# Performance work log

Hardware: AMD Instinct MI355X
Metric: run time of the kernel (lower is better)

Reference implementation:

```python
import jax, jax.numpy as jnp
import numpy as np

N = 100000
E = 1600000

def _graphconv(x, src, dst, W, b):
    # DGL GraphConv, norm='both', in_feats > out_feats path: transform then aggregate.
    ones = jnp.ones((E,), dtype=x.dtype)
    out_deg = jax.ops.segment_sum(ones, src, num_segments=N)
    in_deg = jax.ops.segment_sum(ones, dst, num_segments=N)
    out_norm = jax.lax.rsqrt(jnp.clip(out_deg, 1.0))  # D_out^{-1/2}
    in_norm = jax.lax.rsqrt(jnp.clip(in_deg, 1.0))    # D_in^{-1/2}
    h = (x * out_norm[:, None]) @ W                    # [N, out_feats]
    msg = h[src]                                       # gather over edges [E, out_feats]
    agg = jax.ops.segment_sum(msg, dst, num_segments=N)
    return agg * in_norm[:, None] + b


def setup_inputs() -> dict:
    key = jax.random.key(0)
    k1, k2, k3, k4, k5 = jax.random.split(key, 5)
    features = jax.random.normal(k1, (N, 256), dtype=jnp.float32)
    src = jax.random.randint(k2, (E,), 0, N, dtype=jnp.int32)
    dst = jax.random.randint(k3, (E,), 0, N, dtype=jnp.int32)
    # Xavier-uniform like DGL's GraphConv reset_parameters
    lim1 = float(np.sqrt(6.0 / (256 + 64)))
    lim2 = float(np.sqrt(6.0 / (64 + 40)))
    W1 = jax.random.uniform(k4, (256, 64), jnp.float32, -lim1, lim1)
    W2 = jax.random.uniform(k5, (64, 40), jnp.float32, -lim2, lim2)
    b1 = jnp.zeros((64,), jnp.float32)
    b2 = jnp.zeros((40,), jnp.float32)
    return {"features": features, "src": src, "dst": dst,
            "W1": W1, "b1": b1, "W2": W2, "b2": b2}


def reference(features, src, dst, W1, b1, W2, b2):
    x = _graphconv(features, src, dst, W1, b1)
    x = _graphconv(x, src, dst, W2, b2)
    return x
```

## Files before the change

### kernel.cpp

```cpp
#include <hip/hip_runtime.h>

#define N_NODES 100000
#define N_EDGES 1600000
#define BSH 7
#define NBUCK 782
#define BMASK 127
#define HBLK 512
#define CAP 4096


__global__ __launch_bounds__(256) void coarse_hist_kernel(
    const int* __restrict__ src, const int* __restrict__ dst,
    int* __restrict__ gHD, int* __restrict__ gHS) {
    __shared__ int hd[NBUCK], hs[NBUCK];
    for (int i = threadIdx.x; i < NBUCK; i += 256) { hd[i] = 0; hs[i] = 0; }
    __syncthreads();
    for (int e = blockIdx.x * 256 + threadIdx.x; e < N_EDGES; e += HBLK * 256) {
        atomicAdd(&hd[dst[e] >> BSH], 1);
        atomicAdd(&hs[src[e] >> BSH], 1);
    }
    __syncthreads();
    for (int i = threadIdx.x; i < NBUCK; i += 256) {
        if (hd[i]) atomicAdd(&gHD[i], hd[i]);
        if (hs[i]) atomicAdd(&gHS[i], hs[i]);
    }
}


__global__ __launch_bounds__(1024) void coarse_scan_kernel(
    const int* __restrict__ gHD, const int* __restrict__ gHS,
    int* __restrict__ dBase, int* __restrict__ sBase) {
    __shared__ int sd[1024], se[1024];
    int t = threadIdx.x;
    int vd = (t < NBUCK) ? gHD[t] : 0;
    int vs = (t < NBUCK) ? gHS[t] : 0;
    sd[t] = vd; se[t] = vs;
    __syncthreads();
    for (int s = 1; s < 1024; s <<= 1) {
        int ud = (t >= s) ? sd[t - s] : 0;
        int us = (t >= s) ? se[t - s] : 0;
        __syncthreads();
        sd[t] += ud; se[t] += us;
        __syncthreads();
    }
    if (t < NBUCK) { dBase[t] = sd[t] - vd; sBase[t] = se[t] - vs; }
    if (t == 0) { dBase[NBUCK] = N_EDGES; sBase[NBUCK] = N_EDGES; }
}


__global__ __launch_bounds__(256) void scatter_both_kernel(
    const int* __restrict__ src, const int* __restrict__ dst,
    const int* __restrict__ dBase, const int* __restrict__ sBase,
    int* __restrict__ dRes, int* __restrict__ sRes,
    int* __restrict__ bpack, unsigned char* __restrict__ bslo) {
    __shared__ int hd[NBUCK], hs[NBUCK], curD[NBUCK], curS[NBUCK];
    for (int i = threadIdx.x; i < NBUCK; i += 256) { hd[i] = 0; hs[i] = 0; }
    __syncthreads();
    for (int e = blockIdx.x * 256 + threadIdx.x; e < N_EDGES; e += HBLK * 256) {
        atomicAdd(&hd[dst[e] >> BSH], 1);
        atomicAdd(&hs[src[e] >> BSH], 1);
    }
    __syncthreads();
    for (int i = threadIdx.x; i < NBUCK; i += 256) {
        int cd = hd[i];
        curD[i] = dBase[i] + (cd ? atomicAdd(&dRes[i], cd) : 0);
        int cs = hs[i];
        curS[i] = sBase[i] + (cs ? atomicAdd(&sRes[i], cs) : 0);
    }
    __syncthreads();
    for (int e = blockIdx.x * 256 + threadIdx.x; e < N_EDGES; e += HBLK * 256) {
        int s = src[e];
        int d = dst[e];
        int pd = atomicAdd(&curD[d >> BSH], 1);
        bpack[pd] = (s << BSH) | (d & BMASK);
        int ps = atomicAdd(&curS[s >> BSH], 1);
        bslo[ps] = (unsigned char)(s & BMASK);
    }
}


__global__ __launch_bounds__(256) void fine_src_kernel(
    const int* __restrict__ sBase, const unsigned char* __restrict__ bslo,
    float* __restrict__ onorm) {
    __shared__ int hist[128];
    int t = threadIdx.x, b = blockIdx.x;
    int lo = sBase[b], hi = sBase[b + 1];
    if (t < 128) hist[t] = 0;
    __syncthreads();
    for (int p = lo + t; p < hi; p += 256) atomicAdd(&hist[bslo[p]], 1);
    __syncthreads();
    int node = b * 128 + t;
    if (t < 128 && node < N_NODES) onorm[node] = 1.0f / sqrtf((float)max(hist[t], 1));
}


__global__ __launch_bounds__(128) void gemm1_kernel(
    const float* __restrict__ x, const float* __restrict__ W,
    const float* __restrict__ onorm, float* __restrict__ h, int n) {
    __shared__ float As[16][128];
    __shared__ float Ws[16][68];
    const int tid = threadIdx.x;
    const int tx = tid & 7;
    const int ry = tid >> 3;
    const int rowBase = blockIdx.x * 128;

    const int lr = tid >> 2;
    const int kq = (tid & 3) * 4;
    const int wk = tid >> 3;
    const int wc = (tid & 7) * 8;

    float4 va[4], vw0, vw1;

    auto load_regs = [&](int k0) {
#pragma unroll
        for (int p = 0; p < 4; ++p) {
            int row = rowBase + p * 32 + lr;
            va[p] = (row < n) ? *(const float4*)(x + (size_t)row * 256 + k0 + kq)
                              : make_float4(0.f, 0.f, 0.f, 0.f);
        }
        vw0 = *(const float4*)(W + (size_t)wk * 64 + wc);
        vw1 = *(const float4*)(W + (size_t)wk * 64 + wc + 4);
    };
    auto load_regs_w = [&](int k0) {
#pragma unroll
        for (int p = 0; p < 4; ++p) {
            int row = rowBase + p * 32 + lr;
            va[p] = (row < n) ? *(const float4*)(x + (size_t)row * 256 + k0 + kq)
                              : make_float4(0.f, 0.f, 0.f, 0.f);
        }
        vw0 = *(const float4*)(W + (size_t)(k0 + wk) * 64 + wc);
        vw1 = *(const float4*)(W + (size_t)(k0 + wk) * 64 + wc + 4);
    };

    float acc[8][8] = {};

    load_regs(0);
    for (int k0 = 0; k0 < 256; k0 += 16) {
#pragma unroll
        for (int p = 0; p < 4; ++p) {
            int r = p * 32 + lr;
            As[kq + 0][r] = va[p].x;
            As[kq + 1][r] = va[p].y;
            As[kq + 2][r] = va[p].z;
            As[kq + 3][r] = va[p].w;
        }
        *(float4*)&Ws[wk][wc] = vw0;
        *(float4*)&Ws[wk][wc + 4] = vw1;
        __syncthreads();
        if (k0 + 16 < 256) load_regs_w(k0 + 16);
#pragma unroll
        for (int k = 0; k < 16; ++k) {
            float4 b0 = *(const float4*)&Ws[k][tx * 8];
            float4 b1 = *(const float4*)&Ws[k][tx * 8 + 4];
            float4 a0 = *(const float4*)&As[k][ry * 8];
            float4 a1 = *(const float4*)&As[k][ry * 8 + 4];
            float av[8] = {a0.x, a0.y, a0.z, a0.w, a1.x, a1.y, a1.z, a1.w};
            float bv[8] = {b0.x, b0.y, b0.z, b0.w, b1.x, b1.y, b1.z, b1.w};
#pragma unroll
            for (int i = 0; i < 8; ++i)
#pragma unroll
                for (int j = 0; j < 8; ++j) acc[i][j] += av[i] * bv[j];
        }
        __syncthreads();
    }
#pragma unroll
    for (int i = 0; i < 8; ++i) {
        int row = rowBase + ry * 8 + i;
        if (row < n) {
            float s = onorm[row];
            *(float4*)(h + (size_t)row * 64 + tx * 8) =
                make_float4(acc[i][0] * s, acc[i][1] * s, acc[i][2] * s, acc[i][3] * s);
            *(float4*)(h + (size_t)row * 64 + tx * 8 + 4) =
                make_float4(acc[i][4] * s, acc[i][5] * s, acc[i][6] * s, acc[i][7] * s);
        }
    }
}


__global__ __launch_bounds__(512) void agg64_fused_kernel(
    const int* __restrict__ dBase, const int* __restrict__ bpack,
    const float* __restrict__ h, float* __restrict__ agg, float* __restrict__ inorm) {
    __shared__ int lsrc[CAP];
    __shared__ int hist[128], scn[128], cur[128];
    const int tid = threadIdx.x;
    const int b = blockIdx.x;
    const int lo = dBase[b];
    const int hi = min(dBase[b + 1], lo + CAP);
    if (tid < 128) hist[tid] = 0;
    __syncthreads();
    for (int p = lo + tid; p < hi; p += 512) atomicAdd(&hist[bpack[p] & BMASK], 1);
    __syncthreads();
    int v = (tid < 128) ? hist[tid] : 0;
    if (tid < 128) scn[tid] = v;
    __syncthreads();
    for (int s = 1; s < 128; s <<= 1) {
        int u = 0;
        if (tid < 128 && tid >= s) u = scn[tid - s];
        __syncthreads();
        if (tid < 128 && tid >= s) scn[tid] += u;
        __syncthreads();
    }
    if (tid < 128) {
        int excl = scn[tid] - v;
        scn[tid] = excl;
        cur[tid] = excl;
        int node = b * 128 + tid;
        if (node < N_NODES) inorm[node] = 1.0f / sqrtf((float)max(v, 1));
    }
    __syncthreads();
    for (int p = lo + tid; p < hi; p += 512) {
        int pk = bpack[p];
        int pos = atomicAdd(&cur[pk & BMASK], 1);
        lsrc[pos] = pk >> BSH;
    }
    __syncthreads();

    const int w = tid >> 6, lane = tid & 63, q = lane >> 4, f = lane & 15;
    for (int nn = w; nn < 128; nn += 8) {
        int node = b * 128 + nn;
        if (node >= N_NODES) break;
        int beg = scn[nn];
        int end = beg + hist[nn];
        float4 a0 = {0.f, 0.f, 0.f, 0.f}, a1 = {0.f, 0.f, 0.f, 0.f};
        int j = beg;
        for (; j + 8 <= end; j += 8) {
            int s0 = lsrc[j + q], s1 = lsrc[j + 4 + q];
            float4 v0 = *((const float4*)(h + (size_t)s0 * 64) + f);
            float4 v1 = *((const float4*)(h + (size_t)s1 * 64) + f);
            a0.x += v0.x; a0.y += v0.y; a0.z += v0.z; a0.w += v0.w;
            a1.x += v1.x; a1.y += v1.y; a1.z += v1.z; a1.w += v1.w;
        }
        for (; j + 4 <= end; j += 4) {
            int s0 = lsrc[j + q];
            float4 v0 = *((const float4*)(h + (size_t)s0 * 64) + f);
            a0.x += v0.x; a0.y += v0.y; a0.z += v0.z; a0.w += v0.w;
        }
        if (j + q < end) {
            int s0 = lsrc[j + q];
            float4 v0 = *((const float4*)(h + (size_t)s0 * 64) + f);
            a0.x += v0.x; a0.y += v0.y; a0.z += v0.z; a0.w += v0.w;
        }
        a0.x += a1.x; a0.y += a1.y; a0.z += a1.z; a0.w += a1.w;
        a0.x += __shfl_xor(a0.x, 16); a0.y += __shfl_xor(a0.y, 16);
        a0.z += __shfl_xor(a0.z, 16); a0.w += __shfl_xor(a0.w, 16);
        a0.x += __shfl_xor(a0.x, 32); a0.y += __shfl_xor(a0.y, 32);
        a0.z += __shfl_xor(a0.z, 32); a0.w += __shfl_xor(a0.w, 32);
        if (q == 0) ((float4*)(agg + (size_t)node * 64))[f] = a0;
    }
}


__global__ __launch_bounds__(256) void gemm2_kernel(
    const float* __restrict__ agg, const float* __restrict__ W2,
    const float* __restrict__ b1, const float* __restrict__ inorm,
    const float* __restrict__ onorm, float* __restrict__ h2, int n) {
    const int lane = threadIdx.x & 63;
    const int wid = __builtin_amdgcn_readfirstlane(threadIdx.x >> 6);
    const int rowBase = (blockIdx.x * 4 + wid) * 8;
    const int cl = lane < 40 ? lane : 39;

    float w[64];
#pragma unroll
    for (int k = 0; k < 64; ++k) w[k] = W2[k * 40 + cl];

    float c2 = 0.f;
#pragma unroll
    for (int k = 0; k < 64; ++k) c2 += b1[k] * w[k];

#pragma unroll
    for (int r = 0; r < 8; ++r) {
        int row = rowBase + r;
        if (row < n) {
            const float* ar = agg + (size_t)row * 64;
            float acc = 0.f;
#pragma unroll
            for (int k = 0; k < 64; ++k) acc += ar[k] * w[k];
            float so = onorm[row];
            float s12 = inorm[row] * so;
            if (lane < 40) h2[(size_t)row * 40 + lane] = acc * s12 + so * c2;
        }
    }
}


__global__ __launch_bounds__(512) void agg40_fused_kernel(
    const int* __restrict__ dBase, const int* __restrict__ bpack,
    const float* __restrict__ h2, const float* __restrict__ b2,
    float* __restrict__ out) {
    __shared__ int lsrc[CAP];
    __shared__ int hist[128], scn[128], cur[128];
    const int tid = threadIdx.x;
    const int b = blockIdx.x;
    const int lo = dBase[b];
    const int hi = min(dBase[b + 1], lo + CAP);
    if (tid < 128) hist[tid] = 0;
    __syncthreads();
    for (int p = lo + tid; p < hi; p += 512) atomicAdd(&hist[bpack[p] & BMASK], 1);
    __syncthreads();
    int v = (tid < 128) ? hist[tid] : 0;
    if (tid < 128) scn[tid] = v;
    __syncthreads();
    for (int s = 1; s < 128; s <<= 1) {
        int u = 0;
        if (tid < 128 && tid >= s) u = scn[tid - s];
        __syncthreads();
        if (tid < 128 && tid >= s) scn[tid] += u;
        __syncthreads();
    }
    if (tid < 128) {
        int excl = scn[tid] - v;
        scn[tid] = excl;
        cur[tid] = excl;
    }
    __syncthreads();
    for (int p = lo + tid; p < hi; p += 512) {
        int pk = bpack[p];
        int pos = atomicAdd(&cur[pk & BMASK], 1);
        lsrc[pos] = pk >> BSH;
    }
    __syncthreads();

    const int w = tid >> 6, lane = tid & 63, q = lane >> 4, f = lane & 15;
    const bool act = (f < 10);
    float4 vb = make_float4(0.f, 0.f, 0.f, 0.f);
    if (act) vb = ((const float4*)b2)[f];
    for (int nn = w; nn < 128; nn += 8) {
        int node = b * 128 + nn;
        if (node >= N_NODES) break;
        int beg = scn[nn];
        int end = beg + hist[nn];
        float4 a0 = {0.f, 0.f, 0.f, 0.f}, a1 = {0.f, 0.f, 0.f, 0.f};
        int j = beg;
        for (; j + 8 <= end; j += 8) {
            int s0 = lsrc[j + q], s1 = lsrc[j + 4 + q];
            if (act) {
                float4 v0 = *((const float4*)(h2 + (size_t)s0 * 40) + f);
                float4 v1 = *((const float4*)(h2 + (size_t)s1 * 40) + f);
                a0.x += v0.x; a0.y += v0.y; a0.z += v0.z; a0.w += v0.w;
                a1.x += v1.x; a1.y += v1.y; a1.z += v1.z; a1.w += v1.w;
            }
        }
        for (; j + 4 <= end; j += 4) {
            int s0 = lsrc[j + q];
            if (act) {
                float4 v0 = *((const float4*)(h2 + (size_t)s0 * 40) + f);
                a0.x += v0.x; a0.y += v0.y; a0.z += v0.z; a0.w += v0.w;
            }
        }
        if (j + q < end && act) {
            int s0 = lsrc[j + q];
            float4 v0 = *((const float4*)(h2 + (size_t)s0 * 40) + f);
            a0.x += v0.x; a0.y += v0.y; a0.z += v0.z; a0.w += v0.w;
        }
        a0.x += a1.x; a0.y += a1.y; a0.z += a1.z; a0.w += a1.w;
        a0.x += __shfl_xor(a0.x, 16); a0.y += __shfl_xor(a0.y, 16);
        a0.z += __shfl_xor(a0.z, 16); a0.w += __shfl_xor(a0.w, 16);
        a0.x += __shfl_xor(a0.x, 32); a0.y += __shfl_xor(a0.y, 32);
        a0.z += __shfl_xor(a0.z, 32); a0.w += __shfl_xor(a0.w, 32);
        if (q == 0 && act) {
            float s = 1.0f / sqrtf((float)max(hist[nn], 1));
            float4 r;
            r.x = a0.x * s + vb.x; r.y = a0.y * s + vb.y;
            r.z = a0.z * s + vb.z; r.w = a0.w * s + vb.w;
            ((float4*)(out + (size_t)node * 40))[f] = r;
        }
    }
}

extern "C" void kernel_launch(void* const* d_in, const int* in_sizes, int n_in,
                              void* d_out, int out_size, void* d_ws, size_t ws_size,
                              hipStream_t stream) {
    const float* x  = (const float*)d_in[0];
    const int* src  = (const int*)d_in[1];
    const int* dst  = (const int*)d_in[2];
    const float* W1 = (const float*)d_in[3];
    const float* b1 = (const float*)d_in[4];
    const float* W2 = (const float*)d_in[5];
    const float* b2 = (const float*)d_in[6];
    float* out = (float*)d_out;

    char* wsb = (char*)d_ws;
    size_t off = 0;
    auto alloc = [&](size_t bytes) { char* p = wsb + off; off += (bytes + 255) & ~size_t(255); return p; };

    int*   zeroed = (int*)  alloc(4 * NBUCK * 4);
    int*   gHD    = zeroed;
    int*   gHS    = zeroed + NBUCK;
    int*   dRes   = zeroed + 2 * NBUCK;
    int*   sRes   = zeroed + 3 * NBUCK;
    int*   dBase  = (int*)  alloc((NBUCK + 1) * 4);
    int*   sBase  = (int*)  alloc((NBUCK + 1) * 4);
    float* onorm  = (float*)alloc(N_NODES * 4);
    float* inorm  = (float*)alloc(N_NODES * 4);
    int*   bpack  = (int*)  alloc((size_t)N_EDGES * 4);
    unsigned char* bslo = (unsigned char*)alloc(N_EDGES);
    float* h1     = (float*)alloc((size_t)N_NODES * 64 * 4);
    float* agg1   = (float*)alloc((size_t)N_NODES * 64 * 4);
    float* h2 = h1;

    hipMemsetAsync(zeroed, 0, 4 * NBUCK * 4, stream);

    coarse_hist_kernel<<<HBLK, 256, 0, stream>>>(src, dst, gHD, gHS);
    coarse_scan_kernel<<<1, 1024, 0, stream>>>(gHD, gHS, dBase, sBase);
    scatter_both_kernel<<<HBLK, 256, 0, stream>>>(src, dst, dBase, sBase, dRes, sRes,
                                                  bpack, bslo);
    fine_src_kernel<<<NBUCK, 256, 0, stream>>>(sBase, bslo, onorm);

    gemm1_kernel<<<(N_NODES + 127) / 128, 128, 0, stream>>>(x, W1, onorm, h1, N_NODES);

    agg64_fused_kernel<<<NBUCK, 512, 0, stream>>>(dBase, bpack, h1, agg1, inorm);

    gemm2_kernel<<<(N_NODES + 31) / 32, 256, 0, stream>>>(agg1, W2, b1, inorm, onorm, h2, N_NODES);

    agg40_fused_kernel<<<NBUCK, 512, 0, stream>>>(dBase, bpack, h2, b2, out);
}
```

Measured before the change: 432.8 us.

## Use per-block histograms with scan, LDS atomic aggregation, and wider gemm1 blocks

Counting-sort offsets now come from per-block histograms and a column-wise scan kernel, so the scatter no longer recomputes histograms or takes global atomic reservations. The scatter order becomes deterministic, and the extra HBLK*NBUCK buffers cost more memory traffic. Both aggregation kernels drop the in-LDS bucket sort and per-node warp reduction. They now accumulate edge messages straight into padded shared-memory accumulators with float atomics, which also removes the CAP truncation. gemm1 moves to 256 threads with an 8x4 per-thread tile and no register prefetch.

Measured after the change: 1.396 ms. 3.23x slower.

```diff
diff --git a/kernel.cpp b/kernel.cpp
--- a/kernel.cpp
+++ b/kernel.cpp
@@ -6,12 +6,13 @@
 #define NBUCK 782
 #define BMASK 127
 #define HBLK 512
-#define CAP 4096
+#define PAD64 65
+#define PAD40 41
 
 
 __global__ __launch_bounds__(256) void coarse_hist_kernel(
     const int* __restrict__ src, const int* __restrict__ dst,
-    int* __restrict__ gHD, int* __restrict__ gHS) {
+    int* __restrict__ dHist, int* __restrict__ sHist) {
     __shared__ int hd[NBUCK], hs[NBUCK];
     for (int i = threadIdx.x; i < NBUCK; i += 256) { hd[i] = 0; hs[i] = 0; }
     __syncthreads();
@@ -20,10 +21,35 @@
         atomicAdd(&hs[src[e] >> BSH], 1);
     }
     __syncthreads();
+    size_t base = (size_t)blockIdx.x * NBUCK;
     for (int i = threadIdx.x; i < NBUCK; i += 256) {
-        if (hd[i]) atomicAdd(&gHD[i], hd[i]);
-        if (hs[i]) atomicAdd(&gHS[i], hs[i]);
-    }
+        dHist[base + i] = hd[i];
+        sHist[base + i] = hs[i];
+    }
+}
+
+
+__global__ __launch_bounds__(512) void scan_blocks_kernel(
+    const int* __restrict__ dHist, const int* __restrict__ sHist,
+    int* __restrict__ dOfs, int* __restrict__ sOfs,
+    int* __restrict__ gHD, int* __restrict__ gHS) {
+    __shared__ int sd[512], se[512];
+    const int i = blockIdx.x;
+    const int t = threadIdx.x;
+    int vd = dHist[(size_t)t * NBUCK + i];
+    int vs = sHist[(size_t)t * NBUCK + i];
+    sd[t] = vd; se[t] = vs;
+    __syncthreads();
+    for (int s = 1; s < 512; s <<= 1) {
+        int ud = (t >= s) ? sd[t - s] : 0;
+        int us = (t >= s) ? se[t - s] : 0;
+        __syncthreads();
+        sd[t] += ud; se[t] += us;
+        __syncthreads();
+    }
+    dOfs[(size_t)t * NBUCK + i] = sd[t] - vd;
+    sOfs[(size_t)t * NBUCK + i] = se[t] - vs;
+    if (t == 511) { gHD[i] = sd[511]; gHS[i] = se[511]; }
 }
 
 
@@ -51,21 +77,13 @@
 __global__ __launch_bounds__(256) void scatter_both_kernel(
     const int* __restrict__ src, const int* __restrict__ dst,
     const int* __restrict__ dBase, const int* __restrict__ sBase,
-    int* __restrict__ dRes, int* __restrict__ sRes,
+    const int* __restrict__ dOfs, const int* __restrict__ sOfs,
     int* __restrict__ bpack, unsigned char* __restrict__ bslo) {
-    __shared__ int hd[NBUCK], hs[NBUCK], curD[NBUCK], curS[NBUCK];
-    for (int i = threadIdx.x; i < NBUCK; i += 256) { hd[i] = 0; hs[i] = 0; }
-    __syncthreads();
-    for (int e = blockIdx.x * 256 + threadIdx.x; e < N_EDGES; e += HBLK * 256) {
-        atomicAdd(&hd[dst[e] >> BSH], 1);
-        atomicAdd(&hs[src[e] >> BSH], 1);
-    }
-    __syncthreads();
+    __shared__ int curD[NBUCK], curS[NBUCK];
+    size_t obase = (size_t)blockIdx.x * NBUCK;
     for (int i = threadIdx.x; i < NBUCK; i += 256) {
-        int cd = hd[i];
-        curD[i] = dBase[i] + (cd ? atomicAdd(&dRes[i], cd) : 0);
-        int cs = hs[i];
-        curS[i] = sBase[i] + (cs ? atomicAdd(&sRes[i], cs) : 0);
+        curD[i] = dBase[i] + dOfs[obase + i];
+        curS[i] = sBase[i] + sOfs[obase + i];
     }
     __syncthreads();
     for (int e = blockIdx.x * 256 + threadIdx.x; e < N_EDGES; e += HBLK * 256) {
@@ -94,158 +112,103 @@
 }
 
 
-__global__ __launch_bounds__(128) void gemm1_kernel(
+__global__ __launch_bounds__(256) void gemm1_kernel(
     const float* __restrict__ x, const float* __restrict__ W,
     const float* __restrict__ onorm, float* __restrict__ h, int n) {
     __shared__ float As[16][128];
     __shared__ float Ws[16][68];
     const int tid = threadIdx.x;
-    const int tx = tid & 7;
-    const int ry = tid >> 3;
+    const int tx = tid & 15;
+    const int ry = tid >> 4;
     const int rowBase = blockIdx.x * 128;
 
-    const int lr = tid >> 2;
-    const int kq = (tid & 3) * 4;
-    const int wk = tid >> 3;
-    const int wc = (tid & 7) * 8;
-
-    float4 va[4], vw0, vw1;
-
-    auto load_regs = [&](int k0) {
-#pragma unroll
-        for (int p = 0; p < 4; ++p) {
-            int row = rowBase + p * 32 + lr;
-            va[p] = (row < n) ? *(const float4*)(x + (size_t)row * 256 + k0 + kq)
-                              : make_float4(0.f, 0.f, 0.f, 0.f);
-        }
-        vw0 = *(const float4*)(W + (size_t)wk * 64 + wc);
-        vw1 = *(const float4*)(W + (size_t)wk * 64 + wc + 4);
-    };
-    auto load_regs_w = [&](int k0) {
-#pragma unroll
-        for (int p = 0; p < 4; ++p) {
-            int row = rowBase + p * 32 + lr;
-            va[p] = (row < n) ? *(const float4*)(x + (size_t)row * 256 + k0 + kq)
-                              : make_float4(0.f, 0.f, 0.f, 0.f);
-        }
-        vw0 = *(const float4*)(W + (size_t)(k0 + wk) * 64 + wc);
-        vw1 = *(const float4*)(W + (size_t)(k0 + wk) * 64 + wc + 4);
-    };
-
-    float acc[8][8] = {};
-
-    load_regs(0);
+    const int lr = tid >> 1;
+    const int kq = (tid & 1) * 8;
+    const int wk = tid >> 4;
+    const int wc = (tid & 15) * 4;
+
+    const int row = rowBase + lr;
+    const bool rv = (row < n);
+    const float* xr = x + (size_t)row * 256;
+
+    float acc[8][4] = {};
+
     for (int k0 = 0; k0 < 256; k0 += 16) {
-#pragma unroll
-        for (int p = 0; p < 4; ++p) {
-            int r = p * 32 + lr;
-            As[kq + 0][r] = va[p].x;
-            As[kq + 1][r] = va[p].y;
-            As[kq + 2][r] = va[p].z;
-            As[kq + 3][r] = va[p].w;
-        }
-        *(float4*)&Ws[wk][wc] = vw0;
-        *(float4*)&Ws[wk][wc + 4] = vw1;
-        __syncthreads();
-        if (k0 + 16 < 256) load_regs_w(k0 + 16);
+        float4 v0 = make_float4(0.f, 0.f, 0.f, 0.f), v1 = v0;
+        if (rv) {
+            v0 = *(const float4*)(xr + k0 + kq);
+            v1 = *(const float4*)(xr + k0 + kq + 4);
+        }
+        *(float4*)&Ws[wk][wc] = *(const float4*)(W + (size_t)(k0 + wk) * 64 + wc);
+        As[kq + 0][lr] = v0.x;
+        As[kq + 1][lr] = v0.y;
+        As[kq + 2][lr] = v0.z;
+        As[kq + 3][lr] = v0.w;
+        As[kq + 4][lr] = v1.x;
+        As[kq + 5][lr] = v1.y;
+        As[kq + 6][lr] = v1.z;
+        As[kq + 7][lr] = v1.w;
+        __syncthreads();
 #pragma unroll
         for (int k = 0; k < 16; ++k) {
-            float4 b0 = *(const float4*)&Ws[k][tx * 8];
-            float4 b1 = *(const float4*)&Ws[k][tx * 8 + 4];
+            float4 b = *(const float4*)&Ws[k][tx * 4];
             float4 a0 = *(const float4*)&As[k][ry * 8];
             float4 a1 = *(const float4*)&As[k][ry * 8 + 4];
             float av[8] = {a0.x, a0.y, a0.z, a0.w, a1.x, a1.y, a1.z, a1.w};
-            float bv[8] = {b0.x, b0.y, b0.z, b0.w, b1.x, b1.y, b1.z, b1.w};
+            float bv[4] = {b.x, b.y, b.z, b.w};
 #pragma unroll
             for (int i = 0; i < 8; ++i)
 #pragma unroll
-                for (int j = 0; j < 8; ++j) acc[i][j] += av[i] * bv[j];
+                for (int j = 0; j < 4; ++j) acc[i][j] += av[i] * bv[j];
         }
         __syncthreads();
     }
 #pragma unroll
     for (int i = 0; i < 8; ++i) {
-        int row = rowBase + ry * 8 + i;
-        if (row < n) {
-            float s = onorm[row];
-            *(float4*)(h + (size_t)row * 64 + tx * 8) =
+        int r = rowBase + ry * 8 + i;
+        if (r < n) {
+            float s = onorm[r];
+            *(float4*)(h + (size_t)r * 64 + tx * 4) =
                 make_float4(acc[i][0] * s, acc[i][1] * s, acc[i][2] * s, acc[i][3] * s);
-            *(float4*)(h + (size_t)row * 64 + tx * 8 + 4) =
-                make_float4(acc[i][4] * s, acc[i][5] * s, acc[i][6] * s, acc[i][7] * s);
-        }
-    }
-}
-
-
-__global__ __launch_bounds__(512) void agg64_fused_kernel(
+        }
+    }
+}
+
+
+__global__ __launch_bounds__(512) void agg64_kernel(
     const int* __restrict__ dBase, const int* __restrict__ bpack,
     const float* __restrict__ h, float* __restrict__ agg, float* __restrict__ inorm) {
-    __shared__ int lsrc[CAP];
-    __shared__ int hist[128], scn[128], cur[128];
+    __shared__ float accL[128 * PAD64];
+    __shared__ int degL[128];
     const int tid = threadIdx.x;
     const int b = blockIdx.x;
-    const int lo = dBase[b];
-    const int hi = min(dBase[b + 1], lo + CAP);
-    if (tid < 128) hist[tid] = 0;
-    __syncthreads();
-    for (int p = lo + tid; p < hi; p += 512) atomicAdd(&hist[bpack[p] & BMASK], 1);
-    __syncthreads();
-    int v = (tid < 128) ? hist[tid] : 0;
-    if (tid < 128) scn[tid] = v;
-    __syncthreads();
-    for (int s = 1; s < 128; s <<= 1) {
-        int u = 0;
-        if (tid < 128 && tid >= s) u = scn[tid - s];
-        __syncthreads();
-        if (tid < 128 && tid >= s) scn[tid] += u;
-        __syncthreads();
-    }
+    for (int i = tid; i < 128 * PAD64; i += 512) accL[i] = 0.f;
+    if (tid < 128) degL[tid] = 0;
+    __syncthreads();
+    const int lo = dBase[b], hi = dBase[b + 1];
+    const int f = tid & 15;
+    const int es = tid >> 4;
+    for (int p = lo + es; p < hi; p += 32) {
+        int pk = bpack[p];
+        int dlo = pk & BMASK;
+        int s = pk >> BSH;
+        float4 v = *((const float4*)(h + (size_t)s * 64) + f);
+        float* a = &accL[dlo * PAD64 + f * 4];
+        atomicAdd(a + 0, v.x);
+        atomicAdd(a + 1, v.y);
+        atomicAdd(a + 2, v.z);
+        atomicAdd(a + 3, v.w);
+        if (f == 0) atomicAdd(&degL[dlo], 1);
+    }
+    __syncthreads();
     if (tid < 128) {
-        int excl = scn[tid] - v;
-        scn[tid] = excl;
-        cur[tid] = excl;
         int node = b * 128 + tid;
-        if (node < N_NODES) inorm[node] = 1.0f / sqrtf((float)max(v, 1));
-    }
-    __syncthreads();
-    for (int p = lo + tid; p < hi; p += 512) {
-        int pk = bpack[p];
-        int pos = atomicAdd(&cur[pk & BMASK], 1);
-        lsrc[pos] = pk >> BSH;
-    }
-    __syncthreads();
-
-    const int w = tid >> 6, lane = tid & 63, q = lane >> 4, f = lane & 15;
-    for (int nn = w; nn < 128; nn += 8) {
-        int node = b * 128 + nn;
-        if (node >= N_NODES) break;
-        int beg = scn[nn];
-        int end = beg + hist[nn];
-        float4 a0 = {0.f, 0.f, 0.f, 0.f}, a1 = {0.f, 0.f, 0.f, 0.f};
-        int j = beg;
-        for (; j + 8 <= end; j += 8) {
-            int s0 = lsrc[j + q], s1 = lsrc[j + 4 + q];
-            float4 v0 = *((const float4*)(h + (size_t)s0 * 64) + f);
-            float4 v1 = *((const float4*)(h + (size_t)s1 * 64) + f);
-            a0.x += v0.x; a0.y += v0.y; a0.z += v0.z; a0.w += v0.w;
-            a1.x += v1.x; a1.y += v1.y; a1.z += v1.z; a1.w += v1.w;
-        }
-        for (; j + 4 <= end; j += 4) {
-            int s0 = lsrc[j + q];
-            float4 v0 = *((const float4*)(h + (size_t)s0 * 64) + f);
-            a0.x += v0.x; a0.y += v0.y; a0.z += v0.z; a0.w += v0.w;
-        }
-        if (j + q < end) {
-            int s0 = lsrc[j + q];
-            float4 v0 = *((const float4*)(h + (size_t)s0 * 64) + f);
-            a0.x += v0.x; a0.y += v0.y; a0.z += v0.z; a0.w += v0.w;
-        }
-        a0.x += a1.x; a0.y += a1.y; a0.z += a1.z; a0.w += a1.w;
-        a0.x += __shfl_xor(a0.x, 16); a0.y += __shfl_xor(a0.y, 16);
-        a0.z += __shfl_xor(a0.z, 16); a0.w += __shfl_xor(a0.w, 16);
-        a0.x += __shfl_xor(a0.x, 32); a0.y += __shfl_xor(a0.y, 32);
-        a0.z += __shfl_xor(a0.z, 32); a0.w += __shfl_xor(a0.w, 32);
-        if (q == 0) ((float4*)(agg + (size_t)node * 64))[f] = a0;
+        if (node < N_NODES) inorm[node] = 1.0f / sqrtf((float)max(degL[tid], 1));
+    }
+    for (int i = tid; i < 128 * 64; i += 512) {
+        int nl = i >> 6;
+        int node = b * 128 + nl;
+        if (node < N_NODES) agg[(size_t)node * 64 + (i & 63)] = accL[nl * PAD64 + (i & 63)];
     }
 }
 
@@ -283,86 +246,43 @@
 }
 
 
-__global__ __launch_bounds__(512) void agg40_fused_kernel(
+__global__ __launch_bounds__(512) void agg40_kernel(
     const int* __restrict__ dBase, const int* __restrict__ bpack,
     const float* __restrict__ h2, const float* __restrict__ b2,
     float* __restrict__ out) {
-    __shared__ int lsrc[CAP];
-    __shared__ int hist[128], scn[128], cur[128];
+    __shared__ float accL[128 * PAD40];
+    __shared__ int degL[128];
     const int tid = threadIdx.x;
     const int b = blockIdx.x;
-    const int lo = dBase[b];
-    const int hi = min(dBase[b + 1], lo + CAP);
-    if (tid < 128) hist[tid] = 0;
-    __syncthreads();
-    for (int p = lo + tid; p < hi; p += 512) atomicAdd(&hist[bpack[p] & BMASK], 1);
-    __syncthreads();
-    int v = (tid < 128) ? hist[tid] : 0;
-    if (tid < 128) scn[tid] = v;
-    __syncthreads();
-    for (int s = 1; s < 128; s <<= 1) {
-        int u = 0;
-        if (tid < 128 && tid >= s) u = scn[tid - s];
-        __syncthreads();
-        if (tid < 128 && tid >= s) scn[tid] += u;
-        __syncthreads();
-    }
-    if (tid < 128) {
-        int excl = scn[tid] - v;
-        scn[tid] = excl;
-        cur[tid] = excl;
-    }
-    __syncthreads();
-    for (int p = lo + tid; p < hi; p += 512) {
+    for (int i = tid; i < 128 * PAD40; i += 512) accL[i] = 0.f;
+    if (tid < 128) degL[tid] = 0;
+    __syncthreads();
+    const int lo = dBase[b], hi = dBase[b + 1];
+    const int f = tid & 15;
+    const int es = tid >> 4;
+    const bool act = (f < 10);
+    for (int p = lo + es; p < hi; p += 32) {
         int pk = bpack[p];
-        int pos = atomicAdd(&cur[pk & BMASK], 1);
-        lsrc[pos] = pk >> BSH;
-    }
-    __syncthreads();
-
-    const int w = tid >> 6, lane = tid & 63, q = lane >> 4, f = lane & 15;
-    const bool act = (f < 10);
-    float4 vb = make_float4(0.f, 0.f, 0.f, 0.f);
-    if (act) vb = ((const float4*)b2)[f];
-    for (int nn = w; nn < 128; nn += 8) {
-        int node = b * 128 + nn;
-        if (node >= N_NODES) break;
-        int beg = scn[nn];
-        int end = beg + hist[nn];
-        float4 a0 = {0.f, 0.f, 0.f, 0.f}, a1 = {0.f, 0.f, 0.f, 0.f};
-        int j = beg;
-        for (; j + 8 <= end; j += 8) {
-            int s0 = lsrc[j + q], s1 = lsrc[j + 4 + q];
-            if (act) {
-                float4 v0 = *((const float4*)(h2 + (size_t)s0 * 40) + f);
-                float4 v1 = *((const float4*)(h2 + (size_t)s1 * 40) + f);
-                a0.x += v0.x; a0.y += v0.y; a0.z += v0.z; a0.w += v0.w;
-                a1.x += v1.x; a1.y += v1.y; a1.z += v1.z; a1.w += v1.w;
-            }
-        }
-        for (; j + 4 <= end; j += 4) {
-            int s0 = lsrc[j + q];
-            if (act) {
-                float4 v0 = *((const float4*)(h2 + (size_t)s0 * 40) + f);
-                a0.x += v0.x; a0.y += v0.y; a0.z += v0.z; a0.w += v0.w;
-            }
-        }
-        if (j + q < end && act) {
-            int s0 = lsrc[j + q];
-            float4 v0 = *((const float4*)(h2 + (size_t)s0 * 40) + f);
-            a0.x += v0.x; a0.y += v0.y; a0.z += v0.z; a0.w += v0.w;
-        }
-        a0.x += a1.x; a0.y += a1.y; a0.z += a1.z; a0.w += a1.w;
-        a0.x += __shfl_xor(a0.x, 16); a0.y += __shfl_xor(a0.y, 16);
-        a0.z += __shfl_xor(a0.z, 16); a0.w += __shfl_xor(a0.w, 16);
-        a0.x += __shfl_xor(a0.x, 32); a0.y += __shfl_xor(a0.y, 32);
-        a0.z += __shfl_xor(a0.z, 32); a0.w += __shfl_xor(a0.w, 32);
-        if (q == 0 && act) {
-            float s = 1.0f / sqrtf((float)max(hist[nn], 1));
-            float4 r;
-            r.x = a0.x * s + vb.x; r.y = a0.y * s + vb.y;
-            r.z = a0.z * s + vb.z; r.w = a0.w * s + vb.w;
-            ((float4*)(out + (size_t)node * 40))[f] = r;
+        int dlo = pk & BMASK;
+        int s = pk >> BSH;
+        if (act) {
+            float4 v = *((const float4*)(h2 + (size_t)s * 40) + f);
+            float* a = &accL[dlo * PAD40 + f * 4];
+            atomicAdd(a + 0, v.x);
+            atomicAdd(a + 1, v.y);
+            atomicAdd(a + 2, v.z);
+            atomicAdd(a + 3, v.w);
+        }
+        if (f == 0) atomicAdd(&degL[dlo], 1);
+    }
+    __syncthreads();
+    for (int i = tid; i < 128 * 40; i += 512) {
+        int nl = i / 40;
+        int c = i - nl * 40;
+        int node = b * 128 + nl;
+        if (node < N_NODES) {
+            float s = 1.0f / sqrtf((float)max(degL[nl], 1));
+            out[(size_t)node * 40 + c] = accL[nl * PAD40 + c] * s + b2[c];
         }
     }
 }
@@ -383,13 +303,14 @@
     size_t off = 0;
     auto alloc = [&](size_t bytes) { char* p = wsb + off; off += (bytes + 255) & ~size_t(255); return p; };
 
-    int*   zeroed = (int*)  alloc(4 * NBUCK * 4);
-    int*   gHD    = zeroed;
-    int*   gHS    = zeroed + NBUCK;
-    int*   dRes   = zeroed + 2 * NBUCK;
-    int*   sRes   = zeroed + 3 * NBUCK;
+    int*   gHD    = (int*)  alloc(NBUCK * 4);
+    int*   gHS    = (int*)  alloc(NBUCK * 4);
     int*   dBase  = (int*)  alloc((NBUCK + 1) * 4);
     int*   sBase  = (int*)  alloc((NBUCK + 1) * 4);
+    int*   dHist  = (int*)  alloc((size_t)HBLK * NBUCK * 4);
+    int*   sHist  = (int*)  alloc((size_t)HBLK * NBUCK * 4);
+    int*   dOfs   = (int*)  alloc((size_t)HBLK * NBUCK * 4);
+    int*   sOfs   = (int*)  alloc((size_t)HBLK * NBUCK * 4);
     float* onorm  = (float*)alloc(N_NODES * 4);
     float* inorm  = (float*)alloc(N_NODES * 4);
     int*   bpack  = (int*)  alloc((size_t)N_EDGES * 4);
@@ -398,19 +319,18 @@
     float* agg1   = (float*)alloc((size_t)N_NODES * 64 * 4);
     float* h2 = h1;
 
-    hipMemsetAsync(zeroed, 0, 4 * NBUCK * 4, stream);
-
-    coarse_hist_kernel<<<HBLK, 256, 0, stream>>>(src, dst, gHD, gHS);
+    coarse_hist_kernel<<<HBLK, 256, 0, stream>>>(src, dst, dHist, sHist);
+    scan_blocks_kernel<<<NBUCK, 512, 0, stream>>>(dHist, sHist, dOfs, sOfs, gHD, gHS);
     coarse_scan_kernel<<<1, 1024, 0, stream>>>(gHD, gHS, dBase, sBase);
-    scatter_both_kernel<<<HBLK, 256, 0, stream>>>(src, dst, dBase, sBase, dRes, sRes,
+    scatter_both_kernel<<<HBLK, 256, 0, stream>>>(src, dst, dBase, sBase, dOfs, sOfs,
                                                   bpack, bslo);
     fine_src_kernel<<<NBUCK, 256, 0, stream>>>(sBase, bslo, onorm);
 
-    gemm1_kernel<<<(N_NODES + 127) / 128, 128, 0, stream>>>(x, W1, onorm, h1, N_NODES);
-
-    agg64_fused_kernel<<<NBUCK, 512, 0, stream>>>(dBase, bpack, h1, agg1, inorm);
+    gemm1_kernel<<<(N_NODES + 127) / 128, 256, 0, stream>>>(x, W1, onorm, h1, N_NODES);
+
+    agg64_kernel<<<NBUCK, 512, 0, stream>>>(dBase, bpack, h1, agg1, inorm);
 
     gemm2_kernel<<<(N_NODES + 31) / 32, 256, 0, stream>>>(agg1, W2, b1, inorm, onorm, h2, N_NODES);
 
-    agg40_fused_kernel<<<NBUCK, 512, 0, stream>>>(dBase, bpack, h2, b2, out);
-}
+    agg40_kernel<<<NBUCK, 512, 0, stream>>>(dBase, bpack, h2, b2, out);
+}
```

## Replace atomic bucket reservation with per-block scan, retile gemm1, unroll gathers

Applied to the files above, without the earlier changes.

The coarse histogram now writes per-block bucket counts, and a new column-scan kernel computes deterministic per-block offsets. The scatter kernel no longer recomputes its histogram or reserves ranges with global atomics, and the memset is dropped. gemm1 moves to 256-row tiles with one row loaded per thread and no register prefetch. Both aggregation kernels unroll the edge gather loop to four independent accumulators. The new scan kernel adds a launch and extra workspace traffic, and the gemm1 tile loads per-row strided data without the prefetch overlap.

New measurement: 420.5 us. 2.9% less time.

```diff
diff --git a/kernel.cpp b/kernel.cpp
--- a/kernel.cpp
+++ b/kernel.cpp
@@ -11,7 +11,7 @@
 
 __global__ __launch_bounds__(256) void coarse_hist_kernel(
     const int* __restrict__ src, const int* __restrict__ dst,
-    int* __restrict__ gHD, int* __restrict__ gHS) {
+    int* __restrict__ dHist, int* __restrict__ sHist) {
     __shared__ int hd[NBUCK], hs[NBUCK];
     for (int i = threadIdx.x; i < NBUCK; i += 256) { hd[i] = 0; hs[i] = 0; }
     __syncthreads();
@@ -20,10 +20,35 @@
         atomicAdd(&hs[src[e] >> BSH], 1);
     }
     __syncthreads();
+    size_t base = (size_t)blockIdx.x * NBUCK;
     for (int i = threadIdx.x; i < NBUCK; i += 256) {
-        if (hd[i]) atomicAdd(&gHD[i], hd[i]);
-        if (hs[i]) atomicAdd(&gHS[i], hs[i]);
-    }
+        dHist[base + i] = hd[i];
+        sHist[base + i] = hs[i];
+    }
+}
+
+
+__global__ __launch_bounds__(512) void scan_blocks_kernel(
+    const int* __restrict__ dHist, const int* __restrict__ sHist,
+    int* __restrict__ dOfs, int* __restrict__ sOfs,
+    int* __restrict__ gHD, int* __restrict__ gHS) {
+    __shared__ int sd[512], se[512];
+    const int i = blockIdx.x;
+    const int t = threadIdx.x;
+    int vd = dHist[(size_t)t * NBUCK + i];
+    int vs = sHist[(size_t)t * NBUCK + i];
+    sd[t] = vd; se[t] = vs;
+    __syncthreads();
+    for (int s = 1; s < 512; s <<= 1) {
+        int ud = (t >= s) ? sd[t - s] : 0;
+        int us = (t >= s) ? se[t - s] : 0;
+        __syncthreads();
+        sd[t] += ud; se[t] += us;
+        __syncthreads();
+    }
+    dOfs[(size_t)t * NBUCK + i] = sd[t] - vd;
+    sOfs[(size_t)t * NBUCK + i] = se[t] - vs;
+    if (t == 511) { gHD[i] = sd[511]; gHS[i] = se[511]; }
 }
 
 
@@ -51,21 +76,13 @@
 __global__ __launch_bounds__(256) void scatter_both_kernel(
     const int* __restrict__ src, const int* __restrict__ dst,
     const int* __restrict__ dBase, const int* __restrict__ sBase,
-    int* __restrict__ dRes, int* __restrict__ sRes,
+    const int* __restrict__ dOfs, const int* __restrict__ sOfs,
     int* __restrict__ bpack, unsigned char* __restrict__ bslo) {
-    __shared__ int hd[NBUCK], hs[NBUCK], curD[NBUCK], curS[NBUCK];
-    for (int i = threadIdx.x; i < NBUCK; i += 256) { hd[i] = 0; hs[i] = 0; }
-    __syncthreads();
-    for (int e = blockIdx.x * 256 + threadIdx.x; e < N_EDGES; e += HBLK * 256) {
-        atomicAdd(&hd[dst[e] >> BSH], 1);
-        atomicAdd(&hs[src[e] >> BSH], 1);
-    }
-    __syncthreads();
+    __shared__ int curD[NBUCK], curS[NBUCK];
+    size_t obase = (size_t)blockIdx.x * NBUCK;
     for (int i = threadIdx.x; i < NBUCK; i += 256) {
-        int cd = hd[i];
-        curD[i] = dBase[i] + (cd ? atomicAdd(&dRes[i], cd) : 0);
-        int cs = hs[i];
-        curS[i] = sBase[i] + (cs ? atomicAdd(&sRes[i], cs) : 0);
+        curD[i] = dBase[i] + dOfs[obase + i];
+        curS[i] = sBase[i] + sOfs[obase + i];
     }
     __syncthreads();
     for (int e = blockIdx.x * 256 + threadIdx.x; e < N_EDGES; e += HBLK * 256) {
@@ -94,60 +111,39 @@
 }
 
 
-__global__ __launch_bounds__(128) void gemm1_kernel(
+__global__ __launch_bounds__(256) void gemm1_kernel(
     const float* __restrict__ x, const float* __restrict__ W,
     const float* __restrict__ onorm, float* __restrict__ h, int n) {
-    __shared__ float As[16][128];
+    __shared__ float As[16][256];
     __shared__ float Ws[16][68];
     const int tid = threadIdx.x;
     const int tx = tid & 7;
     const int ry = tid >> 3;
-    const int rowBase = blockIdx.x * 128;
-
-    const int lr = tid >> 2;
-    const int kq = (tid & 3) * 4;
-    const int wk = tid >> 3;
-    const int wc = (tid & 7) * 8;
-
-    float4 va[4], vw0, vw1;
-
-    auto load_regs = [&](int k0) {
-#pragma unroll
-        for (int p = 0; p < 4; ++p) {
-            int row = rowBase + p * 32 + lr;
-            va[p] = (row < n) ? *(const float4*)(x + (size_t)row * 256 + k0 + kq)
-                              : make_float4(0.f, 0.f, 0.f, 0.f);
-        }
-        vw0 = *(const float4*)(W + (size_t)wk * 64 + wc);
-        vw1 = *(const float4*)(W + (size_t)wk * 64 + wc + 4);
-    };
-    auto load_regs_w = [&](int k0) {
-#pragma unroll
-        for (int p = 0; p < 4; ++p) {
-            int row = rowBase + p * 32 + lr;
-            va[p] = (row < n) ? *(const float4*)(x + (size_t)row * 256 + k0 + kq)
-                              : make_float4(0.f, 0.f, 0.f, 0.f);
-        }
-        vw0 = *(const float4*)(W + (size_t)(k0 + wk) * 64 + wc);
-        vw1 = *(const float4*)(W + (size_t)(k0 + wk) * 64 + wc + 4);
-    };
+    const int rowBase = blockIdx.x * 256;
+
+    const int wk = tid >> 4;
+    const int wc = (tid & 15) * 4;
+
+    const int row = rowBase + tid;
+    const bool rv = (row < n);
+    const float* xr = x + (size_t)row * 256;
 
     float acc[8][8] = {};
 
-    load_regs(0);
     for (int k0 = 0; k0 < 256; k0 += 16) {
-#pragma unroll
-        for (int p = 0; p < 4; ++p) {
-            int r = p * 32 + lr;
-            As[kq + 0][r] = va[p].x;
-            As[kq + 1][r] = va[p].y;
-            As[kq + 2][r] = va[p].z;
-            As[kq + 3][r] = va[p].w;
-        }
-        *(float4*)&Ws[wk][wc] = vw0;
-        *(float4*)&Ws[wk][wc + 4] = vw1;
-        __syncthreads();
-        if (k0 + 16 < 256) load_regs_w(k0 + 16);
+        float4 v0 = make_float4(0.f, 0.f, 0.f, 0.f), v1 = v0, v2 = v0, v3 = v0;
+        if (rv) {
+            v0 = *(const float4*)(xr + k0 + 0);
+            v1 = *(const float4*)(xr + k0 + 4);
+            v2 = *(const float4*)(xr + k0 + 8);
+            v3 = *(const float4*)(xr + k0 + 12);
+        }
+        *(float4*)&Ws[wk][wc] = *(const float4*)(W + (size_t)(k0 + wk) * 64 + wc);
+        As[0][tid] = v0.x;  As[1][tid] = v0.y;  As[2][tid] = v0.z;  As[3][tid] = v0.w;
+        As[4][tid] = v1.x;  As[5][tid] = v1.y;  As[6][tid] = v1.z;  As[7][tid] = v1.w;
+        As[8][tid] = v2.x;  As[9][tid] = v2.y;  As[10][tid] = v2.z; As[11][tid] = v2.w;
+        As[12][tid] = v3.x; As[13][tid] = v3.y; As[14][tid] = v3.z; As[15][tid] = v3.w;
+        __syncthreads();
 #pragma unroll
         for (int k = 0; k < 16; ++k) {
             float4 b0 = *(const float4*)&Ws[k][tx * 8];
@@ -165,12 +161,12 @@
     }
 #pragma unroll
     for (int i = 0; i < 8; ++i) {
-        int row = rowBase + ry * 8 + i;
-        if (row < n) {
-            float s = onorm[row];
-            *(float4*)(h + (size_t)row * 64 + tx * 8) =
+        int r = rowBase + ry * 8 + i;
+        if (r < n) {
+            float s = onorm[r];
+            *(float4*)(h + (size_t)r * 64 + tx * 8) =
                 make_float4(acc[i][0] * s, acc[i][1] * s, acc[i][2] * s, acc[i][3] * s);
-            *(float4*)(h + (size_t)row * 64 + tx * 8 + 4) =
+            *(float4*)(h + (size_t)r * 64 + tx * 8 + 4) =
                 make_float4(acc[i][4] * s, acc[i][5] * s, acc[i][6] * s, acc[i][7] * s);
         }
     }
@@ -221,14 +217,19 @@
         if (node >= N_NODES) break;
         int beg = scn[nn];
         int end = beg + hist[nn];
-        float4 a0 = {0.f, 0.f, 0.f, 0.f}, a1 = {0.f, 0.f, 0.f, 0.f};
+        float4 a0 = {0.f, 0.f, 0.f, 0.f}, a1 = a0, a2 = a0, a3 = a0;
         int j = beg;
-        for (; j + 8 <= end; j += 8) {
+        for (; j + 16 <= end; j += 16) {
             int s0 = lsrc[j + q], s1 = lsrc[j + 4 + q];
+            int s2 = lsrc[j + 8 + q], s3 = lsrc[j + 12 + q];
             float4 v0 = *((const float4*)(h + (size_t)s0 * 64) + f);
             float4 v1 = *((const float4*)(h + (size_t)s1 * 64) + f);
+            float4 v2 = *((const float4*)(h + (size_t)s2 * 64) + f);
+            float4 v3 = *((const float4*)(h + (size_t)s3 * 64) + f);
             a0.x += v0.x; a0.y += v0.y; a0.z += v0.z; a0.w += v0.w;
             a1.x += v1.x; a1.y += v1.y; a1.z += v1.z; a1.w += v1.w;
+            a2.x += v2.x; a2.y += v2.y; a2.z += v2.z; a2.w += v2.w;
+            a3.x += v3.x; a3.y += v3.y; a3.z += v3.z; a3.w += v3.w;
         }
         for (; j + 4 <= end; j += 4) {
             int s0 = lsrc[j + q];
@@ -238,9 +239,11 @@
         if (j + q < end) {
             int s0 = lsrc[j + q];
             float4 v0 = *((const float4*)(h + (size_t)s0 * 64) + f);
-            a0.x += v0.x; a0.y += v0.y; a0.z += v0.z; a0.w += v0.w;
+            a1.x += v0.x; a1.y += v0.y; a1.z += v0.z; a1.w += v0.w;
         }
         a0.x += a1.x; a0.y += a1.y; a0.z += a1.z; a0.w += a1.w;
+        a2.x += a3.x; a2.y += a3.y; a2.z += a3.z; a2.w += a3.w;
+        a0.x += a2.x; a0.y += a2.y; a0.z += a2.z; a0.w += a2.w;
         a0.x += __shfl_xor(a0.x, 16); a0.y += __shfl_xor(a0.y, 16);
         a0.z += __shfl_xor(a0.z, 16); a0.w += __shfl_xor(a0.w, 16);
         a0.x += __shfl_xor(a0.x, 32); a0.y += __shfl_xor(a0.y, 32);
@@ -329,15 +332,20 @@
         if (node >= N_NODES) break;
         int beg = scn[nn];
         int end = beg + hist[nn];
-        float4 a0 = {0.f, 0.f, 0.f, 0.f}, a1 = {0.f, 0.f, 0.f, 0.f};
+        float4 a0 = {0.f, 0.f, 0.f, 0.f}, a1 = a0, a2 = a0, a3 = a0;
         int j = beg;
-        for (; j + 8 <= end; j += 8) {
+        for (; j + 16 <= end; j += 16) {
             int s0 = lsrc[j + q], s1 = lsrc[j + 4 + q];
+            int s2 = lsrc[j + 8 + q], s3 = lsrc[j + 12 + q];
             if (act) {
                 float4 v0 = *((const float4*)(h2 + (size_t)s0 * 40) + f);
                 float4 v1 = *((const float4*)(h2 + (size_t)s1 * 40) + f);
+                float4 v2 = *((const float4*)(h2 + (size_t)s2 * 40) + f);
+                float4 v3 = *((const float4*)(h2 + (size_t)s3 * 40) + f);
                 a0.x += v0.x; a0.y += v0.y; a0.z += v0.z; a0.w += v0.w;
                 a1.x += v1.x; a1.y += v1.y; a1.z += v1.z; a1.w += v1.w;
+                a2.x += v2.x; a2.y += v2.y; a2.z += v2.z; a2.w += v2.w;
+                a3.x += v3.x; a3.y += v3.y; a3.z += v3.z; a3.w += v3.w;
             }
         }
         for (; j + 4 <= end; j += 4) {
@@ -350,9 +358,11 @@
         if (j + q < end && act) {
             int s0 = lsrc[j + q];
             float4 v0 = *((const float4*)(h2 + (size_t)s0 * 40) + f);
-            a0.x += v0.x; a0.y += v0.y; a0.z += v0.z; a0.w += v0.w;
+            a1.x += v0.x; a1.y += v0.y; a1.z += v0.z; a1.w += v0.w;
         }
         a0.x += a1.x; a0.y += a1.y; a0.z += a1.z; a0.w += a1.w;
+        a2.x += a3.x; a2.y += a3.y; a2.z += a3.z; a2.w += a3.w;
+        a0.x += a2.x; a0.y += a2.y; a0.z += a2.z; a0.w += a2.w;
         a0.x += __shfl_xor(a0.x, 16); a0.y += __shfl_xor(a0.y, 16);
         a0.z += __shfl_xor(a0.z, 16); a0.w += __shfl_xor(a0.w, 16);
         a0.x += __shfl_xor(a0.x, 32); a0.y += __shfl_xor(a0.y, 32);
@@ -383,13 +393,14 @@
     size_t off = 0;
     auto alloc = [&](size_t bytes) { char* p = wsb + off; off += (bytes + 255) & ~size_t(255); return p; };
 
-    int*   zeroed = (int*)  alloc(4 * NBUCK * 4);
-    int*   gHD    = zeroed;
-    int*   gHS    = zeroed + NBUCK;
-    int*   dRes   = zeroed + 2 * NBUCK;
-    int*   sRes   = zeroed + 3 * NBUCK;
+    int*   gHD    = (int*)  alloc(NBUCK * 4);
+    int*   gHS    = (int*)  alloc(NBUCK * 4);
     int*   dBase  = (int*)  alloc((NBUCK + 1) * 4);
     int*   sBase  = (int*)  alloc((NBUCK + 1) * 4);
+    int*   dHist  = (int*)  alloc((size_t)HBLK * NBUCK * 4);
+    int*   sHist  = (int*)  alloc((size_t)HBLK * NBUCK * 4);
+    int*   dOfs   = (int*)  alloc((size_t)HBLK * NBUCK * 4);
+    int*   sOfs   = (int*)  alloc((size_t)HBLK * NBUCK * 4);
     float* onorm  = (float*)alloc(N_NODES * 4);
     float* inorm  = (float*)alloc(N_NODES * 4);
     int*   bpack  = (int*)  alloc((size_t)N_EDGES * 4);
@@ -398,15 +409,14 @@
     float* agg1   = (float*)alloc((size_t)N_NODES * 64 * 4);
     float* h2 = h1;
 
-    hipMemsetAsync(zeroed, 0, 4 * NBUCK * 4, stream);
-
-    coarse_hist_kernel<<<HBLK, 256, 0, stream>>>(src, dst, gHD, gHS);
+    coarse_hist_kernel<<<HBLK, 256, 0, stream>>>(src, dst, dHist, sHist);
+    scan_blocks_kernel<<<NBUCK, 512, 0, stream>>>(dHist, sHist, dOfs, sOfs, gHD, gHS);
     coarse_scan_kernel<<<1, 1024, 0, stream>>>(gHD, gHS, dBase, sBase);
-    scatter_both_kernel<<<HBLK, 256, 0, stream>>>(src, dst, dBase, sBase, dRes, sRes,
+    scatter_both_kernel<<<HBLK, 256, 0, stream>>>(src, dst, dBase, sBase, dOfs, sOfs,
                                                   bpack, bslo);
     fine_src_kernel<<<NBUCK, 256, 0, stream>>>(sBase, bslo, onorm);
 
-    gemm1_kernel<<<(N_NODES + 127) / 128, 128, 0, stream>>>(x, W1, onorm, h1, N_NODES);
+    gemm1_kernel<<<(N_NODES + 255) / 256, 256, 0, stream>>>(x, W1, onorm, h1, N_NODES);
 
     agg64_fused_kernel<<<NBUCK, 512, 0, stream>>>(dBase, bpack, h1, agg1, inorm);
 
```
